# Kernel tuning notes

Measured on AMD Instinct MI355X. Metric: run time of the kernel, lower is better.

Reference implementation:

```python
import jax, jax.numpy as jnp
import numpy as np

B, S, D = 2, 2048, 2048
H, HKV, DH = 16, 4, 128   # query heads, kv heads, head dim
N_REP = H // HKV
ROPE_BASE = 10000.0


def rotate_half(x):
    x1, x2 = x[..., : DH // 2], x[..., DH // 2 :]
    return jnp.concatenate((-x2, x1), axis=-1)


def rope_tables(seq_len, dtype=jnp.float32):
    inv_freq = 1.0 / (ROPE_BASE ** (jnp.arange(0, DH, 2, dtype=jnp.float32) / DH))
    t = jnp.arange(seq_len, dtype=jnp.float32)
    freqs = jnp.outer(t, inv_freq)                 # [S, DH/2]
    emb = jnp.concatenate((freqs, freqs), axis=-1)  # [S, DH]
    return jnp.cos(emb).astype(dtype), jnp.sin(emb).astype(dtype)


def setup_inputs() -> dict:
    key = jax.random.key(0)
    k1, k2, k3, k4, k5 = jax.random.split(key, 5)
    scale = 1.0 / np.sqrt(D)
    return {
        "hidden_states": jax.random.normal(k1, (B, S, D), dtype=jnp.float32),
        "position_ids": jnp.tile(jnp.arange(S, dtype=jnp.int32)[None, :], (B, 1)),
        "wq": jax.random.normal(k2, (D, H * DH), dtype=jnp.float32) * scale,
        "wk": jax.random.normal(k3, (D, HKV * DH), dtype=jnp.float32) * scale,
        "wv": jax.random.normal(k4, (D, HKV * DH), dtype=jnp.float32) * scale,
        "wo": jax.random.normal(k5, (H * DH, D), dtype=jnp.float32) * scale,
    }


def reference(hidden_states, position_ids, wq, wk, wv, wo):
    x = hidden_states
    b, s, _ = x.shape

    # QKV projections -> [B, H(kv), S, DH]
    q = (x @ wq).reshape(b, s, H, DH).transpose(0, 2, 1, 3)
    k = (x @ wk).reshape(b, s, HKV, DH).transpose(0, 2, 1, 3)
    v = (x @ wv).reshape(b, s, HKV, DH).transpose(0, 2, 1, 3)

    # Rotary position embedding
    cos_t, sin_t = rope_tables(s, x.dtype)
    cos = cos_t[position_ids][:, None, :, :]  # [B,1,S,DH]
    sin = sin_t[position_ids][:, None, :, :]
    q = q * cos + rotate_half(q) * sin
    k = k * cos + rotate_half(k) * sin

    # GQA: repeat KV heads to match query heads
    k = jnp.repeat(k, N_REP, axis=1)  # [B,H,S,DH]
    v = jnp.repeat(v, N_REP, axis=1)

    # Causal SDPA
    scores = jnp.einsum("bhqd,bhkd->bhqk", q, k) / jnp.sqrt(
        jnp.asarray(DH, x.dtype)
    )
    causal = jnp.tril(jnp.ones((s, s), dtype=bool))
    scores = jnp.where(causal[None, None], scores, jnp.asarray(-1e9, x.dtype))
    attn = jax.nn.softmax(scores, axis=-1)
    out = jnp.einsum("bhqk,bhkd->bhqd", attn, v)  # [B,H,S,DH]

    out = out.transpose(0, 2, 1, 3).reshape(b, s, H * DH)
    return out @ wo
```

## Files before the change

kernel.cpp:

```cpp
#include <hip/hip_runtime.h>
#include <cmath>

typedef unsigned short u16;
typedef float floatx4 __attribute__((ext_vector_type(4)));
typedef short short8 __attribute__((ext_vector_type(8)));
typedef short short4v __attribute__((ext_vector_type(4)));
typedef __bf16 bf16x8 __attribute__((ext_vector_type(8)));

#define GLOBAL_AS __attribute__((address_space(1)))
#define LDS_AS __attribute__((address_space(3)))

#define S_LEN 2048
#define D_MODEL 2048
#define NH 16
#define NKV 4
#define DHEAD 128
#define SM_SCALE 0.08838834764831843f
#define K2 (SM_SCALE * 1.4426950408889634f)

__device__ __forceinline__ u16 f2bf(float f) {
    unsigned int u = __builtin_bit_cast(unsigned int, f);
    u += 0x7fffu + ((u >> 16) & 1u);
    return (u16)(u >> 16);
}
__device__ __forceinline__ u16 f2bfr(float f) {
    unsigned int u = __builtin_bit_cast(unsigned int, f);
    return (u16)((u + 0x8000u) >> 16);
}
__device__ __forceinline__ float bf2f(u16 x) {
    unsigned int u = ((unsigned int)x) << 16;
    return __builtin_bit_cast(float, u);
}
__device__ __forceinline__ floatx4 zf4() {
    floatx4 z; z[0] = 0.f; z[1] = 0.f; z[2] = 0.f; z[3] = 0.f; return z;
}
__device__ __forceinline__ floatx4 mfma16(short8 a, short8 b, floatx4 c) {
    return __builtin_amdgcn_mfma_f32_16x16x32_bf16(
        __builtin_bit_cast(bf16x8, a), __builtin_bit_cast(bf16x8, b), c, 0, 0, 0);
}
__device__ __forceinline__ floatx4 mfma16k16(short4v a, short4v b, floatx4 c) {
    return __builtin_amdgcn_mfma_f32_16x16x16bf16_1k(a, b, c, 0, 0, 0);
}
__device__ __forceinline__ void async16(const u16* g, u16* l) {
    __builtin_amdgcn_global_load_lds((GLOBAL_AS void*)g, (LDS_AS void*)l, 16, 0, 0);
}

__global__ void cast_tables_kernel(const float4* __restrict__ in, ushort4* __restrict__ out,
                                   float* __restrict__ cs_tab, float* __restrict__ sn_tab) {
    int bid = blockIdx.x;
    if (bid < 8192) {
        int i = bid * 256 + threadIdx.x;
        float4 v = in[i];
        ushort4 o;
        o.x = f2bf(v.x); o.y = f2bf(v.y); o.z = f2bf(v.z); o.w = f2bf(v.w);
        out[i] = o;
    } else {
        int idx = (bid - 8192) * 256 + threadIdx.x;
        int p = idx >> 6, jj = idx & 63;
        double e = (double)(2 * jj) / 128.0;
        double invf = pow(10000.0, -e);
        float arg = (float)p * (float)invf;
        cs_tab[idx] = (float)cos((double)arg);
        sn_tab[idx] = (float)sin((double)arg);
    }
}

__global__ void transpose_all_kernel(const float* __restrict__ wq, const float* __restrict__ wk,
                                     const float* __restrict__ wv, const float* __restrict__ wo,
                                     u16* __restrict__ Wqkv, u16* __restrict__ Wo) {
    __shared__ float tile[32][33];
    int x = blockIdx.x;
    const float* in; u16* out; int C, bx;
    if (x < 64)      { in = wq; out = Wqkv;                     C = 2048; bx = x * 32; }
    else if (x < 80) { in = wk; out = Wqkv + (size_t)2048*2048; C = 512;  bx = (x - 64) * 32; }
    else if (x < 96) { in = wv; out = Wqkv + (size_t)2560*2048; C = 512;  bx = (x - 80) * 32; }
    else             { in = wo; out = Wo;                       C = 2048; bx = (x - 96) * 32; }
    const int R = 2048;
    int tx = threadIdx.x & 31, ty = threadIdx.x >> 5;
    int by = blockIdx.y * 32;
#pragma unroll
    for (int i = 0; i < 32; i += 8)
        tile[ty + i][tx] = in[(size_t)(by + ty + i) * C + bx + tx];
    __syncthreads();
#pragma unroll
    for (int i = 0; i < 32; i += 8)
        out[(size_t)(bx + ty + i) * R + by + tx] = f2bf(tile[tx][ty + i]);
}

__global__ void rope_k_kernel(u16* __restrict__ Kb, const int* __restrict__ pos,
                              const float4* __restrict__ cs_tab,
                              const float4* __restrict__ sn_tab) {
    int idx = blockIdx.x * 256 + threadIdx.x;
    int j4 = idx & 15;
    int s = (idx >> 4) & 2047;
    int r = idx >> 15;
    int hh = r & 3, b = r >> 2;
    int p = pos[b * S_LEN + s];
    float4 cs = cs_tab[p * 16 + j4];
    float4 sn = sn_tab[p * 16 + j4];
    u16* base = Kb + (((size_t)(b * NKV + hh)) * S_LEN + s) * DHEAD + j4 * 4;
    ushort4 a = *(const ushort4*)(base);
    ushort4 c = *(const ushort4*)(base + 64);
    ushort4 oa, oc;
    float x1, x2;
    x1 = bf2f(a.x); x2 = bf2f(c.x); oa.x = f2bf(x1 * cs.x - x2 * sn.x); oc.x = f2bf(x2 * cs.x + x1 * sn.x);
    x1 = bf2f(a.y); x2 = bf2f(c.y); oa.y = f2bf(x1 * cs.y - x2 * sn.y); oc.y = f2bf(x2 * cs.y + x1 * sn.y);
    x1 = bf2f(a.z); x2 = bf2f(c.z); oa.z = f2bf(x1 * cs.z - x2 * sn.z); oc.z = f2bf(x2 * cs.z + x1 * sn.z);
    x1 = bf2f(a.w); x2 = bf2f(c.w); oa.w = f2bf(x1 * cs.w - x2 * sn.w); oc.w = f2bf(x2 * cs.w + x1 * sn.w);
    *(ushort4*)(base) = oa;
    *(ushort4*)(base + 64) = oc;
}

template <int M_REP>
__device__ __forceinline__ void gemm_mainloop8(const u16* __restrict__ A,
                                               const u16* __restrict__ Bt,
                                               int K,
                                               u16* ldsA0, u16* ldsB0,
                                               u16* ldsA1, u16* ldsB1,
                                               floatx4 acc[M_REP][4]) {
    const int t = threadIdx.x;
    const int lane = t & 63, wave = t >> 6;
    const int wr = wave >> 2, wc = wave & 3;
    const int lr = lane & 15, q = lane >> 4;
    const int swz = lr & 7;
    const int m0 = blockIdx.y * (M_REP * 32), n0 = blockIdx.x * 256;

#pragma unroll
    for (int r = 0; r < M_REP; ++r)
#pragma unroll
        for (int c = 0; c < 4; ++c) acc[r][c] = zf4();

    auto stage = [&](int kt, u16* la, u16* lb) {
        const int k0 = kt * 64;
#pragma unroll
        for (int i = 0; i < M_REP / 2; ++i) {
            int ci = i * 512 + t;
            int row = ci >> 3;
            int kc = ((ci & 7) ^ (row & 7)) << 3;
            async16(A + (size_t)(m0 + row) * K + k0 + kc, la + (i * 512 + wave * 64) * 8);
        }
#pragma unroll
        for (int i = 0; i < 4; ++i) {
            int ci = i * 512 + t;
            int row = ci >> 3;
            int kc = ((ci & 7) ^ (row & 7)) << 3;
            async16(Bt + (size_t)(n0 + row) * K + k0 + kc, lb + (i * 512 + wave * 64) * 8);
        }
    };

    auto compute = [&](const u16* la, const u16* lb) {
        short8 bfr[4][2];
#pragma unroll
        for (int c = 0; c < 4; ++c)
#pragma unroll
            for (int ks = 0; ks < 2; ++ks)
                bfr[c][ks] = *(const short8*)(lb + (wc * 64 + c * 16 + lr) * 64 +
                                              (((ks * 4 + q) ^ swz) << 3));
#pragma unroll
        for (int p = 0; p < M_REP / 2; ++p) {
            short8 af[2][2];
#pragma unroll
            for (int rr2 = 0; rr2 < 2; ++rr2)
#pragma unroll
                for (int ks = 0; ks < 2; ++ks)
                    af[rr2][ks] = *(const short8*)(la + (wr * (M_REP * 16) +
                                                   (2 * p + rr2) * 16 + lr) * 64 +
                                                   (((ks * 4 + q) ^ swz) << 3));
            __builtin_amdgcn_s_setprio(1);
#pragma unroll
            for (int rr2 = 0; rr2 < 2; ++rr2)
#pragma unroll
                for (int c = 0; c < 4; ++c)
#pragma unroll
                    for (int ks = 0; ks < 2; ++ks)
                        acc[2 * p + rr2][c] =
                            mfma16(af[rr2][ks], bfr[c][ks], acc[2 * p + rr2][c]);
            __builtin_amdgcn_s_setprio(0);
        }
    };

    auto waitN = [&]() {
        if constexpr (M_REP == 8) asm volatile("s_waitcnt vmcnt(8)" ::: "memory");
        else                      asm volatile("s_waitcnt vmcnt(6)" ::: "memory");
    };

    const int NT = K / 64;
    stage(0, ldsA0, ldsB0);
    for (int kt = 0; kt < NT; kt += 2) {
        stage(kt + 1, ldsA1, ldsB1);
        waitN();
        __builtin_amdgcn_s_barrier();
        compute(ldsA0, ldsB0);
        __builtin_amdgcn_s_barrier();
        stage(kt + 2 < NT ? kt + 2 : 0, ldsA0, ldsB0);
        waitN();
        __builtin_amdgcn_s_barrier();
        compute(ldsA1, ldsB1);
        __builtin_amdgcn_s_barrier();
    }
    asm volatile("s_waitcnt vmcnt(0)" ::: "memory");
}

__global__ __launch_bounds__(512, 1) void qkv_gemm_kernel(const u16* __restrict__ A,
                                                          const u16* __restrict__ Bt,
                                                          u16* __restrict__ Qb,
                                                          u16* __restrict__ Kb,
                                                          u16* __restrict__ Vt) {
    __shared__ u16 ldsA[2][256 * 64];
    __shared__ u16 ldsB[2][256 * 64];
    floatx4 acc[8][4];
    gemm_mainloop8<8>(A, Bt, D_MODEL, ldsA[0], ldsB[0], ldsA[1], ldsB[1], acc);

    const int t = threadIdx.x, lane = t & 63, wave = t >> 6;
    const int wr = wave >> 2, wc = wave & 3, lr = lane & 15, q = lane >> 4;
    const int m0 = blockIdx.y * 256 + wr * 128, n0 = blockIdx.x * 256 + wc * 64;
#pragma unroll
    for (int r = 0; r < 8; ++r)
#pragma unroll
        for (int c = 0; c < 4; ++c) {
            int gc = n0 + c * 16 + lr;
#pragma unroll
            for (int rr = 0; rr < 4; ++rr) {
                int grow = m0 + r * 16 + q * 4 + rr;
                int bb = grow >> 11, s = grow & 2047;
                u16 bv = f2bf(acc[r][c][rr]);
                int d = gc & 127;
                if (gc < 2048) {
                    int hh = gc >> 7;
                    Qb[(((size_t)(bb * NH + hh)) * S_LEN + s) * DHEAD + d] = bv;
                } else if (gc < 2560) {
                    int hh = (gc - 2048) >> 7;
                    Kb[(((size_t)(bb * NKV + hh)) * S_LEN + s) * DHEAD + d] = bv;
                } else {
                    int hh = (gc - 2560) >> 7;
                    int s2 = s ^ ((d & 8) >> 1);
                    Vt[(((size_t)(bb * NKV + hh)) * DHEAD + d) * S_LEN + s2] = bv;
                }
            }
        }
}

__global__ __launch_bounds__(512, 1) void out_gemm_kernel(const u16* __restrict__ A,
                                                          const u16* __restrict__ Bt,
                                                          float* __restrict__ out) {
    __shared__ u16 ldsA[2][128 * 64];
    __shared__ u16 ldsB[2][256 * 64];
    floatx4 acc[4][4];
    gemm_mainloop8<4>(A, Bt, D_MODEL, ldsA[0], ldsB[0], ldsA[1], ldsB[1], acc);

    const int t = threadIdx.x, lane = t & 63, wave = t >> 6;
    const int wr = wave >> 2, wc = wave & 3, lr = lane & 15, q = lane >> 4;
    const int m0 = blockIdx.y * 128 + wr * 64, n0 = blockIdx.x * 256 + wc * 64;
#pragma unroll
    for (int r = 0; r < 4; ++r)
#pragma unroll
        for (int c = 0; c < 4; ++c) {
            int gc = n0 + c * 16 + lr;
#pragma unroll
            for (int rr = 0; rr < 4; ++rr) {
                int grow = m0 + r * 16 + q * 4 + rr;
                out[(size_t)grow * D_MODEL + gc] = acc[r][c][rr];
            }
        }
}

__global__ __launch_bounds__(256, 2) void fa_kernel(const u16* __restrict__ Qb,
                                                    const u16* __restrict__ Kb,
                                                    const u16* __restrict__ Vt,
                                                    u16* __restrict__ Ob,
                                                    const int* __restrict__ pos,
                                                    const float4* __restrict__ cs_tab,
                                                    const float4* __restrict__ sn_tab) {
    __shared__ u16 ldsK[2][64 * 128];
    __shared__ u16 ldsV[2][128 * 64];

    const int t = threadIdx.x, lane = t & 63, wave = t >> 6;
    const int lr = lane & 15, q = lane >> 4;
    const int swz = lr & 7;

    const int bid = blockIdx.x;
    const int bh = bid >> 4, p = bid & 15;
    const int qt0 = p, qt1 = 31 - p;
    const int b = bh >> 4, h = bh & 15;
    const int kvh = h >> 2;

    const u16* Kp = Kb + (size_t)(b * NKV + kvh) * S_LEN * DHEAD;
    const u16* Vp = Vt + (size_t)(b * NKV + kvh) * DHEAD * S_LEN;

    short8 qf0[4], qf1[4];
    auto load_rope_q = [&](int qt, short8 (&qf)[4]) {
        const u16* Qp = Qb + ((size_t)((b * NH + h) * S_LEN) + qt * 64 + wave * 16) * DHEAD;
#pragma unroll
        for (int kk = 0; kk < 4; ++kk)
            qf[kk] = *(const short8*)(Qp + (size_t)lr * DHEAD + kk * 32 + q * 8);
        const int srow = qt * 64 + wave * 16 + lr;
        const int pp = pos[b * S_LEN + srow];
#pragma unroll
        for (int kk = 0; kk < 2; ++kk)
#pragma unroll
            for (int h4 = 0; h4 < 2; ++h4) {
                float4 cs = cs_tab[pp * 16 + kk * 8 + q * 2 + h4];
                float4 sn = sn_tab[pp * 16 + kk * 8 + q * 2 + h4];
#pragma unroll
                for (int e = 0; e < 4; ++e) {
                    float cc = (&cs.x)[e], ss = (&sn.x)[e];
                    int ei = h4 * 4 + e;
                    float x1 = bf2f((u16)qf[kk][ei]);
                    float x2 = bf2f((u16)qf[kk + 2][ei]);
                    qf[kk][ei]     = (short)f2bf(x1 * cc - x2 * ss);
                    qf[kk + 2][ei] = (short)f2bf(x2 * cc + x1 * ss);
                }
            }
    };
    load_rope_q(qt0, qf0);
    load_rope_q(qt1, qf1);

    auto stage = [&](int kt, int bs) {
#pragma unroll
        for (int i = 0; i < 4; ++i) {
            int ci = i * 256 + t;
            int krow = ci >> 4, kc = ((ci & 15) ^ ((ci >> 4) & 7)) << 3;
            async16(Kp + (size_t)(kt * 64 + krow) * DHEAD + kc,
                    &ldsK[bs][(i * 256 + wave * 64) * 8]);
            int dh = ci >> 3, vc = ((ci & 7) ^ ((ci >> 3) & 7)) << 3;
            async16(Vp + (size_t)dh * S_LEN + kt * 64 + vc,
                    &ldsV[bs][(i * 256 + wave * 64) * 8]);
        }
    };

    floatx4 accO[8];
    float m_i, l_i;

    auto do_tile = [&](int kt, int qt_c, const short8 (&qfc)[4], int bs) {
        floatx4 sc[4];
        __builtin_amdgcn_s_setprio(1);
#pragma unroll
        for (int c = 0; c < 4; ++c) {
            sc[c] = zf4();
#pragma unroll
            for (int kk = 0; kk < 4; ++kk) {
                short8 kfr = *(const short8*)(&ldsK[bs][(c * 16 + lr) * DHEAD +
                                              (((kk * 4 + q) ^ swz) << 3)]);
                sc[c] = mfma16(kfr, qfc[kk], sc[c]);
            }
        }
        __builtin_amdgcn_s_setprio(0);

        if (kt == qt_c) {
            const int qrow = wave * 16 + lr;
#pragma unroll
            for (int c = 0; c < 4; ++c)
#pragma unroll
                for (int rr = 0; rr < 4; ++rr)
                    if (c * 16 + q * 4 + rr > qrow) sc[c][rr] = -3e38f;
        }

        float mx = -3e38f;
#pragma unroll
        for (int c = 0; c < 4; ++c)
#pragma unroll
            for (int rr = 0; rr < 4; ++rr) mx = fmaxf(mx, sc[c][rr]);
        mx = fmaxf(mx, __shfl_xor(mx, 16));
        mx = fmaxf(mx, __shfl_xor(mx, 32));
        float mnew = fmaxf(m_i, mx);
        float mk = mnew * K2;
        bool anyup = __any(mnew > m_i);
        float rs = 0.f;
#pragma unroll
        for (int c = 0; c < 4; ++c)
#pragma unroll
            for (int rr = 0; rr < 4; ++rr) {
                float pe = __builtin_amdgcn_exp2f(fmaf(sc[c][rr], K2, -mk));
                sc[c][rr] = pe;
                rs += pe;
            }
        rs += __shfl_xor(rs, 16);
        rs += __shfl_xor(rs, 32);
        if (anyup) {
            float alpha = __builtin_amdgcn_exp2f(fmaf(m_i, K2, -mk));
            l_i = l_i * alpha + rs;
#pragma unroll
            for (int d = 0; d < 8; ++d) accO[d] *= alpha;
        } else {
            l_i += rs;
        }
        m_i = mnew;

        short4v pb[4];
#pragma unroll
        for (int c = 0; c < 4; ++c) {
            pb[c][0] = (short)f2bfr(sc[c][0]);
            pb[c][1] = (short)f2bfr(sc[c][1]);
            pb[c][2] = (short)f2bfr(sc[c][2]);
            pb[c][3] = (short)f2bfr(sc[c][3]);
        }

        __builtin_amdgcn_s_setprio(1);
#pragma unroll
        for (int ks = 0; ks < 4; ++ks)
#pragma unroll
            for (int d = 0; d < 8; ++d) {
                short4v vf = *(const short4v*)(&ldsV[bs][(d * 16 + lr) * 64 +
                                               (((ks * 2 + (q >> 1)) ^ swz) << 3) +
                                               (((q ^ (lr >> 3)) & 1) << 2)]);
                accO[d] = mfma16k16(vf, pb[ks], accO[d]);
            }
        __builtin_amdgcn_s_setprio(0);
    };

    auto epilogue = [&](int qt_c) {
        const int tok = qt_c * 64 + wave * 16 + lr;
        const float inv = 1.0f / l_i;
        u16* orow = Ob + ((size_t)(b * S_LEN + tok)) * (NH * DHEAD) + h * DHEAD + q * 4;
#pragma unroll
        for (int d = 0; d < 8; ++d) {
            ushort4 o;
            o.x = f2bf(accO[d][0] * inv);
            o.y = f2bf(accO[d][1] * inv);
            o.z = f2bf(accO[d][2] * inv);
            o.w = f2bf(accO[d][3] * inv);
            *(ushort4*)(orow + d * 16) = o;
        }
    };

#pragma unroll
    for (int d = 0; d < 8; ++d) accO[d] = zf4();
    m_i = -3e38f; l_i = 0.f;

    int cur = 0;
    stage(0, 0);
    __syncthreads();

    for (int kt = 0; kt <= qt0; ++kt) {
        int nxt = cur ^ 1;
        int nk = (kt < qt0) ? kt + 1 : 0;
        stage(nk, nxt);
        do_tile(kt, qt0, qf0, cur);
        __syncthreads();
        cur = nxt;
    }
    epilogue(qt0);
#pragma unroll
    for (int d = 0; d < 8; ++d) accO[d] = zf4();
    m_i = -3e38f; l_i = 0.f;

    for (int kt = 0; kt <= qt1; ++kt) {
        int nxt = cur ^ 1;
        if (kt < qt1) stage(kt + 1, nxt);
        do_tile(kt, qt1, qf1, cur);
        __syncthreads();
        cur = nxt;
    }
    epilogue(qt1);
}

extern "C" void kernel_launch(void* const* d_in, const int* in_sizes, int n_in,
                              void* d_out, int out_size, void* d_ws, size_t ws_size,
                              hipStream_t stream) {
    const float* X  = (const float*)d_in[0];
    const int* pos  = (const int*)d_in[1];
    const float* wq = (const float*)d_in[2];
    const float* wk = (const float*)d_in[3];
    const float* wv = (const float*)d_in[4];
    const float* wo = (const float*)d_in[5];
    float* out = (float*)d_out;

    char* w = (char*)d_ws;
    u16* Xbf    = (u16*)(w);
    u16* Wqkv   = (u16*)(w + 16777216);
    u16* Wo     = (u16*)(w + 29360128);
    u16* Qb     = (u16*)(w + 37748736);
    u16* Kb     = (u16*)(w + 54525952);
    u16* Vt     = (u16*)(w + 58720256);
    u16* Ob     = (u16*)(w + 62914560);
    float* cst  = (float*)(w + 79691776);
    float* snt  = (float*)(w + 80216064);

    cast_tables_kernel<<<8704, 256, 0, stream>>>((const float4*)X, (ushort4*)Xbf, cst, snt);
    transpose_all_kernel<<<dim3(160, 64), 256, 0, stream>>>(wq, wk, wv, wo, Wqkv, Wo);
    qkv_gemm_kernel<<<dim3(12, 16), 512, 0, stream>>>(Xbf, Wqkv, Qb, Kb, Vt);
    rope_k_kernel<<<1024, 256, 0, stream>>>(Kb, pos, (const float4*)cst, (const float4*)snt);
    fa_kernel<<<512, 256, 0, stream>>>(Qb, Kb, Vt, Ob, pos, (const float4*)cst, (const float4*)snt);
    out_gemm_kernel<<<dim3(8, 32), 512, 0, stream>>>(Ob, Wo, out);
}
```

Measured before the change: 316.1 us.

## Restructure GEMM mainloop into barrier-separated phases interleaving LDS reads and MFMA

Replaces the two-buffer unrolled GEMM mainloop with a per-k-tile loop that splits the work into quadrant phases. Each phase loads a subset of A/B fragments from LDS and then issues a block of MFMAs, with barriers between phases so waves stay in lockstep and LDS reads can overlap other waves' matrix math. The aim is to hide LDS read latency behind MFMA work, in the style of ping-pong scheduling. The cost is many extra barriers per k-tile, which may stall waves if the phases are unbalanced.

```diff
diff --git a/kernel.cpp b/kernel.cpp
--- a/kernel.cpp
+++ b/kernel.cpp
@@ -112,90 +112,129 @@
 }
 
 template <int M_REP>
-__device__ __forceinline__ void gemm_mainloop8(const u16* __restrict__ A,
-                                               const u16* __restrict__ Bt,
-                                               int K,
-                                               u16* ldsA0, u16* ldsB0,
-                                               u16* ldsA1, u16* ldsB1,
-                                               floatx4 acc[M_REP][4]) {
+__device__ __forceinline__ void gemm_8ph(const u16* __restrict__ A,
+                                         const u16* __restrict__ Bt, int K,
+                                         u16* ldsA, u16* ldsB,
+                                         floatx4 acc[M_REP][4]) {
+    constexpr int BM = M_REP * 32;
+    constexpr int ALOADS = BM / 64;
     const int t = threadIdx.x;
     const int lane = t & 63, wave = t >> 6;
     const int wr = wave >> 2, wc = wave & 3;
     const int lr = lane & 15, q = lane >> 4;
     const int swz = lr & 7;
-    const int m0 = blockIdx.y * (M_REP * 32), n0 = blockIdx.x * 256;
+    const int m0 = blockIdx.y * BM, n0 = blockIdx.x * 256;
 
 #pragma unroll
     for (int r = 0; r < M_REP; ++r)
 #pragma unroll
         for (int c = 0; c < 4; ++c) acc[r][c] = zf4();
 
-    auto stage = [&](int kt, u16* la, u16* lb) {
-        const int k0 = kt * 64;
-#pragma unroll
-        for (int i = 0; i < M_REP / 2; ++i) {
+    auto stageT = [&](int kt, int bs) {
+#pragma unroll
+        for (int i = 0; i < ALOADS; ++i) {
             int ci = i * 512 + t;
-            int row = ci >> 3;
-            int kc = ((ci & 7) ^ (row & 7)) << 3;
-            async16(A + (size_t)(m0 + row) * K + k0 + kc, la + (i * 512 + wave * 64) * 8);
+            int grow = ci >> 3;
+            int kc = ((ci & 7) ^ (grow & 7)) << 3;
+            async16(A + (size_t)(m0 + grow) * K + kt * 64 + kc,
+                    ldsA + bs * (BM * 64) + (i * 512 + wave * 64) * 8);
         }
 #pragma unroll
         for (int i = 0; i < 4; ++i) {
             int ci = i * 512 + t;
-            int row = ci >> 3;
-            int kc = ((ci & 7) ^ (row & 7)) << 3;
-            async16(Bt + (size_t)(n0 + row) * K + k0 + kc, lb + (i * 512 + wave * 64) * 8);
+            int grow = ci >> 3;
+            int kc = ((ci & 7) ^ (grow & 7)) << 3;
+            async16(Bt + (size_t)(n0 + grow) * K + kt * 64 + kc,
+                    ldsB + bs * (256 * 64) + (i * 512 + wave * 64) * 8);
         }
     };
 
-    auto compute = [&](const u16* la, const u16* lb) {
-        short8 bfr[4][2];
-#pragma unroll
-        for (int c = 0; c < 4; ++c)
-#pragma unroll
-            for (int ks = 0; ks < 2; ++ks)
-                bfr[c][ks] = *(const short8*)(lb + (wc * 64 + c * 16 + lr) * 64 +
-                                              (((ks * 4 + q) ^ swz) << 3));
-#pragma unroll
-        for (int p = 0; p < M_REP / 2; ++p) {
-            short8 af[2][2];
-#pragma unroll
-            for (int rr2 = 0; rr2 < 2; ++rr2)
-#pragma unroll
-                for (int ks = 0; ks < 2; ++ks)
-                    af[rr2][ks] = *(const short8*)(la + (wr * (M_REP * 16) +
-                                                   (2 * p + rr2) * 16 + lr) * 64 +
-                                                   (((ks * 4 + q) ^ swz) << 3));
-            __builtin_amdgcn_s_setprio(1);
-#pragma unroll
-            for (int rr2 = 0; rr2 < 2; ++rr2)
-#pragma unroll
-                for (int c = 0; c < 4; ++c)
-#pragma unroll
-                    for (int ks = 0; ks < 2; ++ks)
-                        acc[2 * p + rr2][c] =
-                            mfma16(af[rr2][ks], bfr[c][ks], acc[2 * p + rr2][c]);
-            __builtin_amdgcn_s_setprio(0);
-        }
-    };
-
-    auto waitN = [&]() {
+    const int NT = K / 64;
+    stageT(0, 0);
+
+    for (int kt = 0; kt < NT; ++kt) {
+        const int cur = kt & 1, nxt = cur ^ 1;
+        const int kn = (kt + 1 < NT) ? kt + 1 : 0;
+        const u16* la = ldsA + cur * (BM * 64);
+        const u16* lb = ldsB + cur * (256 * 64);
+        short8 af[M_REP / 2][2], bf[4][2];
+
+        stageT(kn, nxt);
         if constexpr (M_REP == 8) asm volatile("s_waitcnt vmcnt(8)" ::: "memory");
         else                      asm volatile("s_waitcnt vmcnt(6)" ::: "memory");
-    };
-
-    const int NT = K / 64;
-    stage(0, ldsA0, ldsB0);
-    for (int kt = 0; kt < NT; kt += 2) {
-        stage(kt + 1, ldsA1, ldsB1);
-        waitN();
-        __builtin_amdgcn_s_barrier();
-        compute(ldsA0, ldsB0);
-        __builtin_amdgcn_s_barrier();
-        stage(kt + 2 < NT ? kt + 2 : 0, ldsA0, ldsB0);
-        waitN();
-        __builtin_amdgcn_s_barrier();
-        compute(ldsA1, ldsB1);
+        __builtin_amdgcn_s_barrier();
+#pragma unroll
+        for (int nf = 0; nf < 2; ++nf)
+#pragma unroll
+            for (int ks = 0; ks < 2; ++ks)
+                bf[nf][ks] = *(const short8*)(lb + (wc * 64 + nf * 16 + lr) * 64 +
+                                              (((ks * 4 + q) ^ swz) << 3));
+#pragma unroll
+        for (int mf = 0; mf < M_REP / 2; ++mf)
+#pragma unroll
+            for (int ks = 0; ks < 2; ++ks)
+                af[mf][ks] = *(const short8*)(la + (wr * (M_REP * 16) + mf * 16 + lr) * 64 +
+                                              (((ks * 4 + q) ^ swz) << 3));
+        __builtin_amdgcn_s_barrier();
+        __builtin_amdgcn_s_setprio(1);
+#pragma unroll
+        for (int mf = 0; mf < M_REP / 2; ++mf)
+#pragma unroll
+            for (int nf = 0; nf < 2; ++nf)
+#pragma unroll
+                for (int ks = 0; ks < 2; ++ks)
+                    acc[mf][nf] = mfma16(af[mf][ks], bf[nf][ks], acc[mf][nf]);
+        __builtin_amdgcn_s_setprio(0);
+        __builtin_amdgcn_s_barrier();
+
+#pragma unroll
+        for (int nf = 0; nf < 2; ++nf)
+#pragma unroll
+            for (int ks = 0; ks < 2; ++ks)
+                bf[2 + nf][ks] = *(const short8*)(lb + (wc * 64 + (2 + nf) * 16 + lr) * 64 +
+                                                  (((ks * 4 + q) ^ swz) << 3));
+        __builtin_amdgcn_s_barrier();
+        __builtin_amdgcn_s_setprio(1);
+#pragma unroll
+        for (int mf = 0; mf < M_REP / 2; ++mf)
+#pragma unroll
+            for (int nf = 2; nf < 4; ++nf)
+#pragma unroll
+                for (int ks = 0; ks < 2; ++ks)
+                    acc[mf][nf] = mfma16(af[mf][ks], bf[nf][ks], acc[mf][nf]);
+        __builtin_amdgcn_s_setprio(0);
+        __builtin_amdgcn_s_barrier();
+
+#pragma unroll
+        for (int mf = 0; mf < M_REP / 2; ++mf)
+#pragma unroll
+            for (int ks = 0; ks < 2; ++ks)
+                af[mf][ks] = *(const short8*)(la + (wr * (M_REP * 16) +
+                                              (M_REP / 2 + mf) * 16 + lr) * 64 +
+                                              (((ks * 4 + q) ^ swz) << 3));
+        __builtin_amdgcn_s_barrier();
+        __builtin_amdgcn_s_setprio(1);
+#pragma unroll
+        for (int mf = 0; mf < M_REP / 2; ++mf)
+#pragma unroll
+            for (int nf = 0; nf < 2; ++nf)
+#pragma unroll
+                for (int ks = 0; ks < 2; ++ks)
+                    acc[M_REP / 2 + mf][nf] =
+                        mfma16(af[mf][ks], bf[nf][ks], acc[M_REP / 2 + mf][nf]);
+        __builtin_amdgcn_s_setprio(0);
+        __builtin_amdgcn_s_barrier();
+
+        __builtin_amdgcn_s_setprio(1);
+#pragma unroll
+        for (int mf = 0; mf < M_REP / 2; ++mf)
+#pragma unroll
+            for (int nf = 2; nf < 4; ++nf)
+#pragma unroll
+                for (int ks = 0; ks < 2; ++ks)
+                    acc[M_REP / 2 + mf][nf] =
+                        mfma16(af[mf][ks], bf[nf][ks], acc[M_REP / 2 + mf][nf]);
+        __builtin_amdgcn_s_setprio(0);
         __builtin_amdgcn_s_barrier();
     }
     asm volatile("s_waitcnt vmcnt(0)" ::: "memory");
@@ -206,10 +245,10 @@
                                                           u16* __restrict__ Qb,
                                                           u16* __restrict__ Kb,
                                                           u16* __restrict__ Vt) {
-    __shared__ u16 ldsA[2][256 * 64];
-    __shared__ u16 ldsB[2][256 * 64];
+    __shared__ u16 ldsA[2 * 256 * 64];
+    __shared__ u16 ldsB[2 * 256 * 64];
     floatx4 acc[8][4];
-    gemm_mainloop8<8>(A, Bt, D_MODEL, ldsA[0], ldsB[0], ldsA[1], ldsB[1], acc);
+    gemm_8ph<8>(A, Bt, D_MODEL, ldsA, ldsB, acc);
 
     const int t = threadIdx.x, lane = t & 63, wave = t >> 6;
     const int wr = wave >> 2, wc = wave & 3, lr = lane & 15, q = lane >> 4;
@@ -243,10 +282,10 @@
 __global__ __launch_bounds__(512, 1) void out_gemm_kernel(const u16* __restrict__ A,
                                                           const u16* __restrict__ Bt,
                                                           float* __restrict__ out) {
-    __shared__ u16 ldsA[2][128 * 64];
-    __shared__ u16 ldsB[2][256 * 64];
+    __shared__ u16 ldsA[2 * 128 * 64];
+    __shared__ u16 ldsB[2 * 256 * 64];
     floatx4 acc[4][4];
-    gemm_mainloop8<4>(A, Bt, D_MODEL, ldsA[0], ldsB[0], ldsA[1], ldsB[1], acc);
+    gemm_8ph<4>(A, Bt, D_MODEL, ldsA, ldsB, acc);
 
     const int t = threadIdx.x, lane = t & 63, wave = t >> 6;
     const int wr = wave >> 2, wc = wave & 3, lr = lane & 15, q = lane >> 4;
```

Result: slower. 340.6 us (+7.8%).
